# Optimization experiments

Hardware: AMD Instinct MI355X
Metric: run time of the kernel (lower is better)

The kernel has to match this reference:

```python
import jax, jax.numpy as jnp
import numpy as np

N = 100000       # nodes
E = 3200000      # edges (avg degree 32)
IN_F = 256
OUT_F = 128


def setup_inputs() -> dict:
    key = jax.random.key(0)
    k1, k2, k3, k4, k5, k6 = jax.random.split(key, 6)
    x = jax.random.normal(k1, (N, IN_F), dtype=jnp.float32)
    adj_row = jax.random.randint(k2, (E,), 0, N, dtype=jnp.int64)
    adj_col = jax.random.randint(k3, (E,), 0, N, dtype=jnp.int64)
    adj_val = jax.random.uniform(k4, (E,), dtype=jnp.float32)
    stdv = 1.0 / np.sqrt(OUT_F)
    weight = jax.random.uniform(k5, (IN_F, OUT_F), dtype=jnp.float32, minval=-stdv, maxval=stdv)
    bias = jax.random.uniform(k6, (OUT_F,), dtype=jnp.float32, minval=-stdv, maxval=stdv)
    return {"x": x, "adj_row": adj_row, "adj_col": adj_col,
            "adj_val": adj_val, "weight": weight, "bias": bias}


def reference(x, adj_row, adj_col, adj_val, weight, bias):
    # dropout with p=0 is identity
    support = x @ weight                                   # [N, OUT_F] dense GEMM
    # spmm(adj, support): gather neighbor rows, scale by edge value, segment-sum into rows
    gathered = adj_val[:, None] * support[adj_col]         # [E, OUT_F]
    out = jax.ops.segment_sum(gathered, adj_row, num_segments=N)  # [N, OUT_F]
    return jax.nn.relu(out + bias)
```

## Files before the change

kernel.cpp:

```cpp
#include <hip/hip_runtime.h>

#define N_NODES 100000
#define IN_F 256
#define OUT_F 128
#define RPB 64
#define RSHIFT 6
#define NB 1563
#define CAPG 2432
#define CHUNK_SC 8192

typedef short bf16x8 __attribute__((ext_vector_type(8)));
typedef float f32x4  __attribute__((ext_vector_type(4)));

static __device__ __forceinline__ unsigned short f2bf(float f) {
    unsigned int u = __float_as_uint(f);
    u = (u + 0x7FFF + ((u >> 16) & 1)) >> 16;
    return (unsigned short)u;
}

__global__ __launch_bounds__(256) void wt_kernel(const float* __restrict__ w,
                                                 unsigned short* __restrict__ wT,
                                                 int* __restrict__ gcur) {
    int n = blockIdx.x;
    int k = threadIdx.x;
    wT[n * IN_F + k] = f2bf(w[(size_t)k * OUT_F + n]);
    if (blockIdx.x < 7) {
        int i = blockIdx.x * 256 + threadIdx.x;
        if (i < NB) gcur[i] = i * CAPG;
    }
}

__global__ __launch_bounds__(256) void gemm_mfma_kernel(const float* __restrict__ x,
                                                        const unsigned short* __restrict__ wT,
                                                        unsigned short* __restrict__ supb) {
    __shared__ unsigned short A_lds[32][264];

    const int tid  = threadIdx.x;
    const int wave = tid >> 6;
    const int lane = tid & 63;
    const int quad = lane >> 4;
    const int l15  = lane & 15;
    const int row_base = blockIdx.x * 32;

    bf16x8 bfrag[2][8];
    {
        const unsigned short* wb = wT + (size_t)(wave * 32 + l15) * IN_F + quad * 8;
#pragma unroll
        for (int ct = 0; ct < 2; ++ct)
#pragma unroll
            for (int ks = 0; ks < 8; ++ks)
                bfrag[ct][ks] = *(const bf16x8*)(wb + ct * 16 * IN_F + ks * 32);
    }

    {
        const float* xb = x + (size_t)row_base * IN_F;
#pragma unroll
        for (int i = 0; i < 8; ++i) {
            int fidx = i * 1024 + tid * 4;
            float4 a = *(const float4*)(xb + fidx);
            int r = fidx >> 8;
            int c = fidx & 255;
            ushort4 u = {f2bf(a.x), f2bf(a.y), f2bf(a.z), f2bf(a.w)};
            *(ushort4*)&A_lds[r][c] = u;
        }
    }
    __syncthreads();

    f32x4 acc[2][2];
#pragma unroll
    for (int rt = 0; rt < 2; ++rt)
#pragma unroll
        for (int ct = 0; ct < 2; ++ct) acc[rt][ct] = (f32x4){0.f, 0.f, 0.f, 0.f};

#pragma unroll
    for (int ks = 0; ks < 8; ++ks) {
        bf16x8 a0 = *(const bf16x8*)&A_lds[l15][ks * 32 + quad * 8];
        bf16x8 a1 = *(const bf16x8*)&A_lds[16 + l15][ks * 32 + quad * 8];
        acc[0][0] = __builtin_amdgcn_mfma_f32_16x16x32_bf16(a0, bfrag[0][ks], acc[0][0], 0, 0, 0);
        acc[0][1] = __builtin_amdgcn_mfma_f32_16x16x32_bf16(a0, bfrag[1][ks], acc[0][1], 0, 0, 0);
        acc[1][0] = __builtin_amdgcn_mfma_f32_16x16x32_bf16(a1, bfrag[0][ks], acc[1][0], 0, 0, 0);
        acc[1][1] = __builtin_amdgcn_mfma_f32_16x16x32_bf16(a1, bfrag[1][ks], acc[1][1], 0, 0, 0);
    }

#pragma unroll
    for (int rt = 0; rt < 2; ++rt)
#pragma unroll
        for (int ct = 0; ct < 2; ++ct)
#pragma unroll
            for (int r = 0; r < 4; ++r) {
                int orow = row_base + rt * 16 + quad * 4 + r;
                int ocol = wave * 32 + ct * 16 + l15;
                supb[(size_t)orow * OUT_F + ocol] = f2bf(acc[rt][ct][r]);
            }
}

__global__ __launch_bounds__(1024) void scatter_kernel(const int* __restrict__ adj_row,
                                                       const int* __restrict__ adj_col,
                                                       const float* __restrict__ adj_val,
                                                       int* __restrict__ gcur,
                                                       int2* __restrict__ ebuf, int E) {
    __shared__ int pref[NB + 1];
    __shared__ int shf[NB];
    __shared__ int2 se[CHUNK_SC];
    __shared__ short sbk[CHUNK_SC];
    __shared__ int wsum[16];

    const int tid  = threadIdx.x;
    const int base = blockIdx.x * CHUNK_SC;
    const int m    = min(CHUNK_SC, E - base);
    const int nv   = m >> 2;

    for (int b = tid; b <= NB; b += 1024) pref[b] = 0;
    __syncthreads();

    for (int j = tid; j < nv; j += 1024) {
        int4 r4 = ((const int4*)(adj_row + base))[j];
        atomicAdd(&pref[r4.x >> RSHIFT], 1);
        atomicAdd(&pref[r4.y >> RSHIFT], 1);
        atomicAdd(&pref[r4.z >> RSHIFT], 1);
        atomicAdd(&pref[r4.w >> RSHIFT], 1);
    }
    if (tid < (m & 3)) atomicAdd(&pref[adj_row[base + (nv << 2) + tid] >> RSHIFT], 1);
    __syncthreads();

    {
        int loc[2];
        const int bb = tid * 2;
        int s = 0;
#pragma unroll
        for (int g = 0; g < 2; ++g) {
            int b = bb + g;
            int v = (b < NB) ? pref[b] : 0;
            loc[g] = s;
            s += v;
        }
        const int lane = tid & 63, wv = tid >> 6;
        int inc = s;
        for (int d = 1; d < 64; d <<= 1) {
            int t = __shfl_up(inc, d, 64);
            if (lane >= d) inc += t;
        }
        if (lane == 63) wsum[wv] = inc;
        __syncthreads();
        int wb2 = 0;
        for (int k = 0; k < wv; ++k) wb2 += wsum[k];
        const int texcl = wb2 + inc - s;
#pragma unroll
        for (int g = 0; g < 2; ++g) {
            int b = bb + g;
            if (b < NB) pref[b] = texcl + loc[g];
        }
        if (tid == 1023) pref[NB] = texcl + s;
    }
    __syncthreads();

    for (int b = tid; b < NB; b += 1024) {
        int s0 = pref[b];
        int c  = pref[b + 1] - s0;
        if (c > 0) shf[b] = atomicAdd(&gcur[b], c) - s0;
    }
    __syncthreads();

    for (int j = tid; j < nv; j += 1024) {
        int4   c4 = ((const int4*)(adj_col + base))[j];
        int4   r4 = ((const int4*)(adj_row + base))[j];
        float4 v4 = ((const float4*)(adj_val + base))[j];
        int p, bk;
        bk = r4.x >> RSHIFT; p = atomicAdd(&pref[bk], 1);
        se[p] = make_int2(c4.x | ((r4.x & (RPB - 1)) << 17), __float_as_int(v4.x)); sbk[p] = (short)bk;
        bk = r4.y >> RSHIFT; p = atomicAdd(&pref[bk], 1);
        se[p] = make_int2(c4.y | ((r4.y & (RPB - 1)) << 17), __float_as_int(v4.y)); sbk[p] = (short)bk;
        bk = r4.z >> RSHIFT; p = atomicAdd(&pref[bk], 1);
        se[p] = make_int2(c4.z | ((r4.z & (RPB - 1)) << 17), __float_as_int(v4.z)); sbk[p] = (short)bk;
        bk = r4.w >> RSHIFT; p = atomicAdd(&pref[bk], 1);
        se[p] = make_int2(c4.w | ((r4.w & (RPB - 1)) << 17), __float_as_int(v4.w)); sbk[p] = (short)bk;
    }
    if (tid < (m & 3)) {
        int i = base + (nv << 2) + tid;
        int r = adj_row[i];
        int bk = r >> RSHIFT;
        int p = atomicAdd(&pref[bk], 1);
        se[p] = make_int2(adj_col[i] | ((r & (RPB - 1)) << 17), __float_as_int(adj_val[i]));
        sbk[p] = (short)bk;
    }
    __syncthreads();

    for (int p = tid; p < m; p += 1024) {
        int bk = sbk[p];
        int g = shf[bk] + p;
        if (g < (bk + 1) * CAPG) ebuf[g] = se[p];
    }
}

__global__ __launch_bounds__(256) void spmm_kernel(const int2* __restrict__ ebuf,
                                                   const int* __restrict__ gcur,
                                                   const unsigned short* __restrict__ supb,
                                                   const float* __restrict__ bias,
                                                   float* __restrict__ out) {
    __shared__ int2 se[CAPG];
    __shared__ int cnt[RPB];
    __shared__ int off[RPB];
    __shared__ int cur[RPB];

    const int tid  = threadIdx.x;
    const int b    = blockIdx.x;
    const int wave = tid >> 6;
    const int lane = tid & 63;
    const int f0   = lane * 2;

    const int start = b * CAPG;
    int m = gcur[b] - start;
    if (m > CAPG) m = CAPG;

    if (tid < RPB) cnt[tid] = 0;
    __syncthreads();

    int2 ev[10];
#pragma unroll
    for (int j = 0; j < 10; ++j) {
        int i = j * 256 + tid;
        if (i < m) {
            ev[j] = ebuf[start + i];
            atomicAdd(&cnt[ev[j].x >> 17], 1);
        }
    }
    __syncthreads();

    if (tid < RPB) {
        int v = cnt[tid];
        int s = v;
#pragma unroll
        for (int d = 1; d < RPB; d <<= 1) {
            int t = __shfl_up(s, d, 64);
            if (tid >= d) s += t;
        }
        off[tid] = s - v;
        cur[tid] = s - v;
    }
    __syncthreads();

#pragma unroll
    for (int j = 0; j < 10; ++j) {
        int i = j * 256 + tid;
        if (i < m) {
            int p = atomicAdd(&cur[ev[j].x >> 17], 1);
            se[p] = ev[j];
        }
    }
    __syncthreads();

    float2 acc[16];
#pragma unroll
    for (int j = 0; j < 16; ++j) acc[j] = make_float2(0.f, 0.f);

#pragma unroll
    for (int j = 0; j < 16; ++j) {
        int r = wave * 16 + j;
        int o = off[r];
        int c = cnt[r];
        float2 a = acc[j];
        int i = 0;
        for (; i + 4 <= c; i += 4) {
            int2 e0 = se[o + i + 0];
            int2 e1 = se[o + i + 1];
            int2 e2 = se[o + i + 2];
            int2 e3 = se[o + i + 3];
            unsigned int u0 = *(const unsigned int*)(supb + (size_t)(e0.x & 0x1FFFF) * OUT_F + f0);
            unsigned int u1 = *(const unsigned int*)(supb + (size_t)(e1.x & 0x1FFFF) * OUT_F + f0);
            unsigned int u2 = *(const unsigned int*)(supb + (size_t)(e2.x & 0x1FFFF) * OUT_F + f0);
            unsigned int u3 = *(const unsigned int*)(supb + (size_t)(e3.x & 0x1FFFF) * OUT_F + f0);
            float v0 = __int_as_float(e0.y), v1 = __int_as_float(e1.y);
            float v2 = __int_as_float(e2.y), v3 = __int_as_float(e3.y);
            a.x += v0 * __uint_as_float(u0 << 16);
            a.y += v0 * __uint_as_float(u0 & 0xFFFF0000u);
            a.x += v1 * __uint_as_float(u1 << 16);
            a.y += v1 * __uint_as_float(u1 & 0xFFFF0000u);
            a.x += v2 * __uint_as_float(u2 << 16);
            a.y += v2 * __uint_as_float(u2 & 0xFFFF0000u);
            a.x += v3 * __uint_as_float(u3 << 16);
            a.y += v3 * __uint_as_float(u3 & 0xFFFF0000u);
        }
        for (; i < c; ++i) {
            int2 e = se[o + i];
            unsigned int u = *(const unsigned int*)(supb + (size_t)(e.x & 0x1FFFF) * OUT_F + f0);
            float v = __int_as_float(e.y);
            a.x += v * __uint_as_float(u << 16);
            a.y += v * __uint_as_float(u & 0xFFFF0000u);
        }
        acc[j] = a;
    }

    float2 bv = *((const float2*)bias + lane);
    const int rbase = b << RSHIFT;
#pragma unroll
    for (int j = 0; j < 16; ++j) {
        int grow = rbase + wave * 16 + j;
        if (grow < N_NODES) {
            float2 o;
            o.x = fmaxf(acc[j].x + bv.x, 0.f);
            o.y = fmaxf(acc[j].y + bv.y, 0.f);
            *((float2*)(out + (size_t)grow * OUT_F) + lane) = o;
        }
    }
}

extern "C" void kernel_launch(void* const* d_in, const int* in_sizes, int n_in,
                              void* d_out, int out_size, void* d_ws, size_t ws_size,
                              hipStream_t stream) {
    const float* x       = (const float*)d_in[0];
    const int*   adj_row = (const int*)d_in[1];
    const int*   adj_col = (const int*)d_in[2];
    const float* adj_val = (const float*)d_in[3];
    const float* weight  = (const float*)d_in[4];
    const float* bias    = (const float*)d_in[5];
    float* out = (float*)d_out;
    const int E = in_sizes[1];

    char* p = (char*)d_ws;
    unsigned short* supb = (unsigned short*)p;  p += (size_t)N_NODES * OUT_F * 2;
    int2* ebuf           = (int2*)p;            p += (size_t)NB * CAPG * 8;
    unsigned short* wT   = (unsigned short*)p;  p += (size_t)OUT_F * IN_F * 2;
    int* gcur            = (int*)p;             p += (size_t)NB * 4;

    wt_kernel<<<OUT_F, 256, 0, stream>>>(weight, wT, gcur);
    gemm_mfma_kernel<<<N_NODES / 32, 256, 0, stream>>>(x, wT, supb);
    scatter_kernel<<<(E + CHUNK_SC - 1) / CHUNK_SC, 1024, 0, stream>>>(adj_row, adj_col,
                                                                       adj_val, gcur, ebuf, E);
    spmm_kernel<<<NB, 256, 0, stream>>>(ebuf, gcur, supb, bias, out);
}
```

Before: 338.5 us.

## Split SpMM wave into four edge groups with 16-byte gathers and shuffle reduction

The SpMM inner loop changes from each lane owning 2 features and walking every edge to four 16-lane quarter-waves that each process a different edge, with each lane loading 8 bf16 features (16 bytes) per edge. Partial sums are combined across quarters with xor shuffles, and the output is written as two float4 stores by the first quarter. This cuts the number of gather instructions per edge and widens memory transactions, but adds a 16-shuffle reduction per row and idles three quarters of the wave during the store.

```diff
diff --git a/kernel.cpp b/kernel.cpp
--- a/kernel.cpp
+++ b/kernel.cpp
@@ -16,6 +16,13 @@
     unsigned int u = __float_as_uint(f);
     u = (u + 0x7FFF + ((u >> 16) & 1)) >> 16;
     return (unsigned short)u;
+}
+
+static __device__ __forceinline__ float bflo(unsigned int u) {
+    return __uint_as_float(u << 16);
+}
+static __device__ __forceinline__ float bfhi(unsigned int u) {
+    return __uint_as_float(u & 0xFFFF0000u);
 }
 
 __global__ __launch_bounds__(256) void wt_kernel(const float* __restrict__ w,
@@ -206,7 +213,9 @@
     const int b    = blockIdx.x;
     const int wave = tid >> 6;
     const int lane = tid & 63;
-    const int f0   = lane * 2;
+    const int q    = lane >> 4;
+    const int l15  = lane & 15;
+    const int fe   = l15 * 8;
 
     const int start = b * CAPG;
     int m = gcur[b] - start;
@@ -249,57 +258,65 @@
     }
     __syncthreads();
 
-    float2 acc[16];
-#pragma unroll
-    for (int j = 0; j < 16; ++j) acc[j] = make_float2(0.f, 0.f);
-
-#pragma unroll
+    const float4 bv0 = ((const float4*)bias)[l15 * 2];
+    const float4 bv1 = ((const float4*)bias)[l15 * 2 + 1];
+    const int rbase = b << RSHIFT;
+
     for (int j = 0; j < 16; ++j) {
-        int r = wave * 16 + j;
-        int o = off[r];
-        int c = cnt[r];
-        float2 a = acc[j];
+        const int r = wave * 16 + j;
+        const int o = off[r];
+        const int c = cnt[r];
+        float a0 = 0.f, a1 = 0.f, a2 = 0.f, a3 = 0.f;
+        float a4 = 0.f, a5 = 0.f, a6 = 0.f, a7 = 0.f;
         int i = 0;
-        for (; i + 4 <= c; i += 4) {
-            int2 e0 = se[o + i + 0];
-            int2 e1 = se[o + i + 1];
-            int2 e2 = se[o + i + 2];
-            int2 e3 = se[o + i + 3];
-            unsigned int u0 = *(const unsigned int*)(supb + (size_t)(e0.x & 0x1FFFF) * OUT_F + f0);
-            unsigned int u1 = *(const unsigned int*)(supb + (size_t)(e1.x & 0x1FFFF) * OUT_F + f0);
-            unsigned int u2 = *(const unsigned int*)(supb + (size_t)(e2.x & 0x1FFFF) * OUT_F + f0);
-            unsigned int u3 = *(const unsigned int*)(supb + (size_t)(e3.x & 0x1FFFF) * OUT_F + f0);
-            float v0 = __int_as_float(e0.y), v1 = __int_as_float(e1.y);
-            float v2 = __int_as_float(e2.y), v3 = __int_as_float(e3.y);
-            a.x += v0 * __uint_as_float(u0 << 16);
-            a.y += v0 * __uint_as_float(u0 & 0xFFFF0000u);
-            a.x += v1 * __uint_as_float(u1 << 16);
-            a.y += v1 * __uint_as_float(u1 & 0xFFFF0000u);
-            a.x += v2 * __uint_as_float(u2 << 16);
-            a.y += v2 * __uint_as_float(u2 & 0xFFFF0000u);
-            a.x += v3 * __uint_as_float(u3 << 16);
-            a.y += v3 * __uint_as_float(u3 & 0xFFFF0000u);
-        }
-        for (; i < c; ++i) {
-            int2 e = se[o + i];
-            unsigned int u = *(const unsigned int*)(supb + (size_t)(e.x & 0x1FFFF) * OUT_F + f0);
+        for (; i + 8 <= c; i += 8) {
+            int2 e0 = se[o + i + q];
+            int2 e1 = se[o + i + 4 + q];
+            uint4 u0 = *(const uint4*)(supb + (size_t)(e0.x & 0x1FFFF) * OUT_F + fe);
+            uint4 u1 = *(const uint4*)(supb + (size_t)(e1.x & 0x1FFFF) * OUT_F + fe);
+            float v0 = __int_as_float(e0.y);
+            float v1 = __int_as_float(e1.y);
+            a0 += v0 * bflo(u0.x); a1 += v0 * bfhi(u0.x);
+            a2 += v0 * bflo(u0.y); a3 += v0 * bfhi(u0.y);
+            a4 += v0 * bflo(u0.z); a5 += v0 * bfhi(u0.z);
+            a6 += v0 * bflo(u0.w); a7 += v0 * bfhi(u0.w);
+            a0 += v1 * bflo(u1.x); a1 += v1 * bfhi(u1.x);
+            a2 += v1 * bflo(u1.y); a3 += v1 * bfhi(u1.y);
+            a4 += v1 * bflo(u1.z); a5 += v1 * bfhi(u1.z);
+            a6 += v1 * bflo(u1.w); a7 += v1 * bfhi(u1.w);
+        }
+        for (int t = i + q; t < c; t += 4) {
+            int2 e = se[o + t];
+            uint4 u = *(const uint4*)(supb + (size_t)(e.x & 0x1FFFF) * OUT_F + fe);
             float v = __int_as_float(e.y);
-            a.x += v * __uint_as_float(u << 16);
-            a.y += v * __uint_as_float(u & 0xFFFF0000u);
-        }
-        acc[j] = a;
-    }
-
-    float2 bv = *((const float2*)bias + lane);
-    const int rbase = b << RSHIFT;
-#pragma unroll
-    for (int j = 0; j < 16; ++j) {
-        int grow = rbase + wave * 16 + j;
-        if (grow < N_NODES) {
-            float2 o;
-            o.x = fmaxf(acc[j].x + bv.x, 0.f);
-            o.y = fmaxf(acc[j].y + bv.y, 0.f);
-            *((float2*)(out + (size_t)grow * OUT_F) + lane) = o;
+            a0 += v * bflo(u.x); a1 += v * bfhi(u.x);
+            a2 += v * bflo(u.y); a3 += v * bfhi(u.y);
+            a4 += v * bflo(u.z); a5 += v * bfhi(u.z);
+            a6 += v * bflo(u.w); a7 += v * bfhi(u.w);
+        }
+        a0 += __shfl_xor(a0, 16); a0 += __shfl_xor(a0, 32);
+        a1 += __shfl_xor(a1, 16); a1 += __shfl_xor(a1, 32);
+        a2 += __shfl_xor(a2, 16); a2 += __shfl_xor(a2, 32);
+        a3 += __shfl_xor(a3, 16); a3 += __shfl_xor(a3, 32);
+        a4 += __shfl_xor(a4, 16); a4 += __shfl_xor(a4, 32);
+        a5 += __shfl_xor(a5, 16); a5 += __shfl_xor(a5, 32);
+        a6 += __shfl_xor(a6, 16); a6 += __shfl_xor(a6, 32);
+        a7 += __shfl_xor(a7, 16); a7 += __shfl_xor(a7, 32);
+
+        const int grow = rbase + r;
+        if (q == 0 && grow < N_NODES) {
+            float* ob = out + (size_t)grow * OUT_F + fe;
+            float4 o0, o1;
+            o0.x = fmaxf(a0 + bv0.x, 0.f);
+            o0.y = fmaxf(a1 + bv0.y, 0.f);
+            o0.z = fmaxf(a2 + bv0.z, 0.f);
+            o0.w = fmaxf(a3 + bv0.w, 0.f);
+            o1.x = fmaxf(a4 + bv1.x, 0.f);
+            o1.y = fmaxf(a5 + bv1.y, 0.f);
+            o1.z = fmaxf(a6 + bv1.z, 0.f);
+            o1.w = fmaxf(a7 + bv1.w, 0.f);
+            *(float4*)ob       = o0;
+            *(float4*)(ob + 4) = o1;
         }
     }
 }
```

Measured after the change: 339.9 us. Within noise of the previous version (+0.4%).
